# Performance work log

Measured on AMD Instinct MI355X. Metric: run time of the kernel, lower is better.

The kernel has to match this reference:

```python
import math
import jax, jax.numpy as jnp
import numpy as np

EPS = 1e-5

def lstm(x, Wih, Whh, b):
    # x: [N,T,D]; PyTorch gate order i,f,g,o; b = b_ih + b_hh combined
    N = x.shape[0]
    H = Whh.shape[1]
    gx = jnp.einsum('ntd,gd->ntg', x, Wih) + b  # [N,T,4H]
    def step(carry, g):
        h, c = carry
        z = g + h @ Whh.T
        i, f, gg, o = jnp.split(z, 4, axis=-1)
        c = jax.nn.sigmoid(f) * c + jax.nn.sigmoid(i) * jnp.tanh(gg)
        h = jax.nn.sigmoid(o) * jnp.tanh(c)
        return (h, c), h
    init = (jnp.zeros((N, H), x.dtype), jnp.zeros((N, H), x.dtype))
    (hN, _), ys = jax.lax.scan(step, init, jnp.swapaxes(gx, 0, 1))
    return jnp.swapaxes(ys, 0, 1), hN  # outputs [N,T,H], h_n [N,H]

def bilstm_layer(x, fW, fU, fb, bW, bU, bb):
    of, _ = lstm(x, fW, fU, fb)
    ob, _ = lstm(x[:, ::-1], bW, bU, bb)
    return jnp.concatenate([of, ob[:, ::-1]], axis=-1)

def layernorm(x, g, b):
    m = jnp.mean(x, -1, keepdims=True)
    v = jnp.mean((x - m) ** 2, -1, keepdims=True)
    return (x - m) * jax.lax.rsqrt(v + EPS) * g + b

def encoder_layer(src, Wq, bq, Wk, bk, Wv, bv, Wo, bo, W1, b1, W2, b2, lng, lnb):
    B, S, d = src.shape
    G, NH = 5, 5
    dk = d // NH
    # group channel shuffle (as in source)
    qs = src.reshape(B, S, G, d // G).swapaxes(-1, -2).reshape(B, S, d)
    q = qs @ Wq.T + bq
    k = q @ Wk.T + bk   # NOTE: source applies W_k/W_v to the projected query
    v = q @ Wv.T + bv
    def heads(t):
        return t.reshape(B, S, NH, dk).transpose(0, 2, 1, 3)
    qh, kh, vh = heads(q), heads(k), heads(v)
    attn = jax.nn.softmax(jnp.einsum('bhqd,bhkd->bhqk', qh, kh) / math.sqrt(dk), axis=-1)
    o = jnp.einsum('bhqk,bhkd->bhqd', attn, vh).transpose(0, 2, 1, 3).reshape(B, S, d)
    o = o @ Wo.T + bo
    src = layernorm(src + o, lng, lnb)          # dropout is identity in eval
    ff = jax.nn.relu(src @ W1.T + b1) @ W2.T + b2
    src = layernorm(src + ff, lng, lnb)         # same LayerNorm params reused
    return src, attn

def _forward(x, qWih, qWhh, qb, kWih, kWhh, kb, vWih, vWhh, vb,
             tWq, tbq, tWk, tbk, tWv, tbv, tWo, tbo, tW1, tb1, tW2, tb2, tlng, tlnb,
             l0fWih, l0fWhh, l0fb, l0bWih, l0bWhh, l0bb,
             l1fWih, l1fWhh, l1fb, l1bWih, l1bWhh, l1bb,
             fc1W, fc1b, fc2W, fc2b):
    B, T, F = x.shape
    H = qWhh.shape[1]
    # per-feature LSTMs: shared weights across features -> batch them
    xf = x.transpose(0, 2, 1).reshape(B * F, T, 1)
    _, hq = lstm(xf, qWih, qWhh, qb)   # [B*F,H]
    _, hk = lstm(xf, kWih, kWhh, kb)   # [B*F,H]
    _, hv = lstm(xf, vWih, vWhh, vb)   # [B*F,1]
    Q = hq.reshape(B, F, H)
    K = hk.reshape(B, F, H)
    V = hv.reshape(B, F)
    # b_ij = (q_i . k_j)/sqrt(H) * v_j, softmax over j
    scores = jnp.einsum('bih,bjh->bij', Q, K) / math.sqrt(H) * V[:, None, :]
    Wsm = jax.nn.softmax(scores, axis=-1)          # [B,F,F] rows indexed by i
    attn_output = jnp.einsum('btj,bij->bti', x, Wsm)  # bmm(x, softmax_b_i)
    b = Wsm.transpose(0, 2, 1)                     # stack(b_list, dim=-1)
    src = jnp.concatenate([x, attn_output], axis=-1)  # [B,T,2F]
    attns = []
    for l in range(2):
        src, a = encoder_layer(src, tWq[l], tbq[l], tWk[l], tbk[l], tWv[l], tbv[l],
                               tWo[l], tbo[l], tW1[l], tb1[l], tW2[l], tb2[l],
                               tlng[l], tlnb[l])
        attns.append(a)
    c = jnp.stack(attns)                           # [2,B,5,T,T]
    out = bilstm_layer(src, l0fWih, l0fWhh, l0fb, l0bWih, l0bWhh, l0bb)
    out = bilstm_layer(out, l1fWih, l1fWhh, l1fb, l1bWih, l1bWhh, l1bb)
    out = jax.nn.relu(out[:, -1, :])               # [B,2H]
    out = jax.nn.relu(out @ fc1W.T + fc1b)
    out = out @ fc2W.T + fc2b                      # [B,1]
    return out, b, c

def setup_inputs() -> dict:
    B, T, F, H = 16, 128, 40, 64
    d = 2 * F
    key = jax.random.key(0)
    ks = iter(jax.random.split(key, 64))
    def n(shape, fan):
        return (jax.random.normal(next(ks), shape) / math.sqrt(fan)).astype(jnp.float32)
    inp = {'x': jax.random.normal(next(ks), (B, T, F), dtype=jnp.float32)}
    # per-feature LSTMs
    inp.update(qWih=n((4 * H, 1), 1), qWhh=n((4 * H, H), H), qb=n((4 * H,), H))
    inp.update(kWih=n((4 * H, 1), 1), kWhh=n((4 * H, H), H), kb=n((4 * H,), H))
    inp.update(vWih=n((4, 1), 1), vWhh=n((4, 1), 1), vb=n((4,), 1))
    # transformer (2 layers stacked on leading axis)
    inp.update(tWq=n((2, d, d), d), tbq=n((2, d), d), tWk=n((2, d, d), d), tbk=n((2, d), d),
               tWv=n((2, d, d), d), tbv=n((2, d), d), tWo=n((2, d, d), d), tbo=n((2, d), d),
               tW1=n((2, 4 * d, d), d), tb1=n((2, 4 * d), d), tW2=n((2, d, 4 * d), 4 * d),
               tb2=n((2, d), 4 * d), tlng=jnp.ones((2, d), jnp.float32), tlnb=jnp.zeros((2, d), jnp.float32))
    # main bidirectional 2-layer LSTM
    inp.update(l0fWih=n((4 * H, d), d), l0fWhh=n((4 * H, H), H), l0fb=n((4 * H,), H),
               l0bWih=n((4 * H, d), d), l0bWhh=n((4 * H, H), H), l0bb=n((4 * H,), H),
               l1fWih=n((4 * H, 2 * H), 2 * H), l1fWhh=n((4 * H, H), H), l1fb=n((4 * H,), H),
               l1bWih=n((4 * H, 2 * H), 2 * H), l1bWhh=n((4 * H, H), H), l1bb=n((4 * H,), H))
    inp.update(fc1W=n((H, 2 * H), 2 * H), fc1b=n((H,), 2 * H), fc2W=n((1, H), H), fc2b=n((1,), H))
    return inp

def reference(x, qWih, qWhh, qb, kWih, kWhh, kb, vWih, vWhh, vb,
              tWq, tbq, tWk, tbk, tWv, tbv, tWo, tbo, tW1, tb1, tW2, tb2, tlng, tlnb,
              l0fWih, l0fWhh, l0fb, l0bWih, l0bWhh, l0bb,
              l1fWih, l1fWhh, l1fb, l1bWih, l1bWhh, l1bb,
              fc1W, fc1b, fc2W, fc2b):
    return _forward(x, qWih, qWhh, qb, kWih, kWhh, kb, vWih, vWhh, vb,
                    tWq, tbq, tWk, tbk, tWv, tbv, tWo, tbo, tW1, tb1, tW2, tb2, tlng, tlnb,
                    l0fWih, l0fWhh, l0fb, l0bWih, l0bWhh, l0bb,
                    l1fWih, l1fWhh, l1fb, l1bWih, l1bWhh, l1bb,
                    fc1W, fc1b, fc2W, fc2b)
```

## Files before the change

### kernel.cpp

```cpp
#include <hip/hip_runtime.h>

__device__ __forceinline__ float sigf(float x){ return 1.0f/(1.0f+__expf(-x)); }
__device__ __forceinline__ float tanhfast(float x){ return 1.0f - 2.0f/(__expf(2.0f*x)+1.0f); }

#define Bn 16
#define Tn 128
#define Fn 40
#define Hn 64
#define Dn 80
#define NHn 5
#define DKn 16
#define FFn 320

#define LOAD_PIN_ROW(dst, srcp)                                        \
  {                                                                    \
    _Pragma("unroll")                                                  \
    for (int jj=0; jj<16; ++jj){                                       \
      float4 tv = *(const float4*)((srcp) + 4*jj);                     \
      dst[4*jj]=tv.x; dst[4*jj+1]=tv.y; dst[4*jj+2]=tv.z; dst[4*jj+3]=tv.w; \
    }                                                                  \
    _Pragma("unroll")                                                  \
    for (int jj=0; jj<64; ++jj){ asm volatile("" : "+v"(dst[jj])); }   \
  }

#define LD4(p,i) (((const float4*)(p))[i])
#define DECL8(v, p) \
  float4 v##0=LD4(p,0), v##1=LD4(p,1), v##2=LD4(p,2), v##3=LD4(p,3), \
         v##4=LD4(p,4), v##5=LD4(p,5), v##6=LD4(p,6), v##7=LD4(p,7);
#define PIN4(P) asm volatile("" : "+v"(P.x), "+v"(P.y), "+v"(P.z), "+v"(P.w));
#define PIN8(v) PIN4(v##0) PIN4(v##1) PIN4(v##2) PIN4(v##3) PIN4(v##4) PIN4(v##5) \
  PIN4(v##6) PIN4(v##7)
#define ACC8(base) \
  { const float4 h0=hb4[(base)+0]; a += h0.x*w0.x + h0.y*w0.y + h0.z*w0.z + h0.w*w0.w; } \
  { const float4 h1=hb4[(base)+1]; a += h1.x*w1.x + h1.y*w1.y + h1.z*w1.z + h1.w*w1.w; } \
  { const float4 h2=hb4[(base)+2]; a += h2.x*w2.x + h2.y*w2.y + h2.z*w2.z + h2.w*w2.w; } \
  { const float4 h3=hb4[(base)+3]; a += h3.x*w3.x + h3.y*w3.y + h3.z*w3.z + h3.w*w3.w; } \
  { const float4 h4=hb4[(base)+4]; a += h4.x*w4.x + h4.y*w4.y + h4.z*w4.z + h4.w*w4.w; } \
  { const float4 h5=hb4[(base)+5]; a += h5.x*w5.x + h5.y*w5.y + h5.z*w5.z + h5.w*w5.w; } \
  { const float4 h6=hb4[(base)+6]; a += h6.x*w6.x + h6.y*w6.y + h6.z*w6.z + h6.w*w6.w; } \
  { const float4 h7=hb4[(base)+7]; a += h7.x*w7.x + h7.y*w7.y + h7.z*w7.z + h7.w*w7.w; }

__global__ __launch_bounds__(128,1) void k_feat_lstm2(
    const float* __restrict__ x,
    const float* __restrict__ qWih, const float* __restrict__ qWhh, const float* __restrict__ qb,
    const float* __restrict__ kWih, const float* __restrict__ kWhh, const float* __restrict__ kb,
    const float* __restrict__ vWih, const float* __restrict__ vWhh, const float* __restrict__ vb,
    float* __restrict__ hq, float* __restrict__ hk, float* __restrict__ hv)
{
  const int blk = blockIdx.x;
  const int l = threadIdx.x;
  if (blk >= 1280){
    const int inst = (blk - 1280)*128 + l;
    const int bi = inst/Fn, f = inst%Fn;
    const float* xp = x + bi*Tn*Fn + f;
    const float wih0=vWih[0], wih1=vWih[1], wih2=vWih[2], wih3=vWih[3];
    const float u0=vWhh[0], u1=vWhh[1], u2=vWhh[2], u3=vWhh[3];
    const float c0=vb[0], c1=vb[1], c2=vb[2], c3=vb[3];
    float h=0.f, c=0.f;
    #pragma unroll 1
    for (int t=0;t<Tn;++t){
      float xt = xp[t*Fn];
      float zi = xt*wih0 + h*u0 + c0;
      float zf = xt*wih1 + h*u1 + c1;
      float zg = xt*wih2 + h*u2 + c2;
      float zo = xt*wih3 + h*u3 + c3;
      c = sigf(zf)*c + sigf(zi)*tanhfast(zg);
      h = sigf(zo)*tanhfast(c);
    }
    hv[inst] = h;
    return;
  }
  const bool isk = blk >= 640;
  const int inst = isk ? blk-640 : blk;
  const int bi = inst/Fn, f = inst%Fn;
  const float* Whh = isk ? kWhh : qWhh;
  const float* Wih = isk ? kWih : qWih;
  const float* bia = isk ? kb  : qb;
  float* outp = isk ? hk : hq;

  const int r0 = l;
  const int r1 = l + 128;

  float w0[Hn], w1[Hn];
  LOAD_PIN_ROW(w0, Whh + r0*Hn);
  LOAD_PIN_ROW(w1, Whh + r1*Hn);
  const float wih0 = Wih[r0], wih1 = Wih[r1];
  const float bb0 = bia[r0], bb1 = bia[r1];

  __shared__ __align__(16) float hb[Hn];
  __shared__ float zb[4*Hn];
  __shared__ float xls[Tn];

  const float* xp = x + bi*Tn*Fn + f;
  xls[l] = xp[l*Fn];
  if (l < Hn) hb[l] = 0.f;
  float c = 0.f, h = 0.f;
  __syncthreads();

  const float4* hb4 = (const float4*)hb;
  #pragma unroll 1
  for (int t=0;t<Tn;++t){
    const float xt = xls[t];
    float a0 = bb0 + xt*wih0;
    float a1 = bb1 + xt*wih1;
    #pragma unroll
    for (int jj=0; jj<16; ++jj){
      const float4 hv4 = hb4[jj];
      a0 += hv4.x*w0[4*jj  ] + hv4.y*w0[4*jj+1] + hv4.z*w0[4*jj+2] + hv4.w*w0[4*jj+3];
      a1 += hv4.x*w1[4*jj  ] + hv4.y*w1[4*jj+1] + hv4.z*w1[4*jj+2] + hv4.w*w1[4*jj+3];
    }
    if (l >= Hn){ zb[l] = a0; zb[l+128] = a1; }
    __syncthreads();
    if (l < Hn){
      const float zi = a0, zg = a1;
      const float zf = zb[l+64], zo = zb[l+192];
      c = sigf(zf)*c + sigf(zi)*tanhfast(zg);
      h = sigf(zo)*tanhfast(c);
      hb[l] = h;
    }
    __syncthreads();
  }
  if (l < Hn) outp[inst*Hn + l] = h;
}

__global__ __launch_bounds__(64) void k_featattn(
    const float* __restrict__ hq, const float* __restrict__ hk, const float* __restrict__ hv,
    float* __restrict__ Wsm, float* __restrict__ out_b)
{
  const int blk = blockIdx.x;
  const int bi = blk / Fn, i = blk % Fn;
  const int j = threadIdx.x;
  __shared__ float qrow[Hn];
  qrow[j] = hq[blk*Hn + j];
  __syncthreads();
  float s = -1e30f;
  if (j < Fn){
    const float* krow = hk + (bi*Fn + j)*Hn;
    float a = 0.f;
    #pragma unroll
    for (int h2=0; h2<Hn; ++h2) a += qrow[h2]*krow[h2];
    s = a * 0.125f * hv[bi*Fn + j];
  }
  float m = s;
  #pragma unroll
  for (int off=32; off>0; off>>=1) m = fmaxf(m, __shfl_xor(m, off));
  float e = (j < Fn) ? __expf(s - m) : 0.f;
  float tot = e;
  #pragma unroll
  for (int off=32; off>0; off>>=1) tot += __shfl_xor(tot, off);
  float p = e / tot;
  if (j < Fn){
    Wsm[blk*Fn + j] = p;
    out_b[bi*(Fn*Fn) + j*Fn + i] = p;
  }
}

__global__ __launch_bounds__(128) void k_build_src(
    const float* __restrict__ x, const float* __restrict__ Wsm, float* __restrict__ src)
{
  const int blk = blockIdx.x;
  const int bi = blk / Tn;
  const int tid = threadIdx.x;
  __shared__ float xrow[Fn];
  if (tid < Fn) xrow[tid] = x[blk*Fn + tid];
  __syncthreads();
  if (tid < Fn){
    src[blk*Dn + tid] = xrow[tid];
  } else if (tid < Dn){
    const int i = tid - Fn;
    const float* wrow = Wsm + (bi*Fn + i)*Fn;
    float a = 0.f;
    #pragma unroll
    for (int j2=0;j2<Fn;++j2) a += xrow[j2]*wrow[j2];
    src[blk*Dn + tid] = a;
  }
}

__global__ __launch_bounds__(128) void k_qkv(
    const float* __restrict__ src,
    const float* __restrict__ Wq, const float* __restrict__ bq,
    const float* __restrict__ Wk, const float* __restrict__ bk,
    const float* __restrict__ Wv, const float* __restrict__ bv,
    float* __restrict__ q, float* __restrict__ k, float* __restrict__ v)
{
  const int row = blockIdx.x;
  const int t = threadIdx.x;
  __shared__ float qs[Dn];
  __shared__ float qrow[Dn];
  if (t < Dn) qs[t] = src[row*Dn + (t%5)*16 + t/5];
  __syncthreads();
  if (t < Dn){
    const float* wr = Wq + t*Dn;
    float a = bq[t];
    #pragma unroll 8
    for (int d2=0; d2<Dn; ++d2) a += qs[d2]*wr[d2];
    qrow[t] = a;
    q[row*Dn + t] = a;
  }
  __syncthreads();
  if (t < Dn){
    const float* wk = Wk + t*Dn;
    const float* wv = Wv + t*Dn;
    float ak = bk[t], av = bv[t];
    #pragma unroll 8
    for (int d2=0; d2<Dn; ++d2){ float qq = qrow[d2]; ak += qq*wk[d2]; av += qq*wv[d2]; }
    k[row*Dn + t] = ak;
    v[row*Dn + t] = av;
  }
}

__global__ __launch_bounds__(128) void k_attn(
    const float* __restrict__ q, const float* __restrict__ k, const float* __restrict__ v,
    float* __restrict__ o, float* __restrict__ c_out)
{
  const int s1 = blockIdx.x, h = blockIdx.y, bi = blockIdx.z;
  const int s2 = threadIdx.x;
  __shared__ float qf[DKn];
  __shared__ float p[Tn];
  __shared__ float pa[128];
  __shared__ float red_m[2];
  __shared__ float red_s[2];
  if (s2 < DKn) qf[s2] = q[(bi*Tn + s1)*Dn + h*DKn + s2];
  __syncthreads();
  const float* krow = k + (bi*Tn + s2)*Dn + h*DKn;
  float a = 0.f;
  #pragma unroll
  for (int d2=0; d2<DKn; ++d2) a += qf[d2]*krow[d2];
  a *= 0.25f;
  const int wv_id = s2 >> 6;
  float m = a;
  #pragma unroll
  for (int off=32; off>0; off>>=1) m = fmaxf(m, __shfl_xor(m, off));
  if ((s2 & 63) == 0) red_m[wv_id] = m;
  __syncthreads();
  m = fmaxf(red_m[0], red_m[1]);
  float e = __expf(a - m);
  float tot = e;
  #pragma unroll
  for (int off=32; off>0; off>>=1) tot += __shfl_xor(tot, off);
  if ((s2 & 63) == 0) red_s[wv_id] = tot;
  __syncthreads();
  tot = red_s[0] + red_s[1];
  float pv = e / tot;
  p[s2] = pv;
  c_out[((bi*NHn + h)*Tn + s1)*Tn + s2] = pv;
  __syncthreads();
  {
    const int d    = s2 & 15;
    const int part = s2 >> 4;
    const float* vcol = v + bi*Tn*Dn + h*DKn + d;
    float acc = 0.f;
    #pragma unroll
    for (int jj=0; jj<16; ++jj){
      const int j2 = part*16 + jj;
      acc += p[j2]*vcol[j2*Dn];
    }
    pa[s2] = acc;
  }
  __syncthreads();
  if (s2 < DKn){
    float acc = 0.f;
    #pragma unroll
    for (int k2=0; k2<8; ++k2) acc += pa[k2*16 + s2];
    o[(bi*Tn + s1)*Dn + h*DKn + s2] = acc;
  }
}

__global__ __launch_bounds__(320) void k_oln_ffln(
    const float* __restrict__ o, const float* __restrict__ Wo, const float* __restrict__ bo,
    const float* __restrict__ W1, const float* __restrict__ b1,
    const float* __restrict__ W2, const float* __restrict__ b2,
    const float* __restrict__ lng, const float* __restrict__ lnb, float* __restrict__ src)
{
  const int row = blockIdx.x;
  const int t = threadIdx.x;
  __shared__ float orow[Dn];
  __shared__ float s1row[Dn];
  __shared__ float h1[FFn];
  __shared__ float red[128];
  if (t < Dn) orow[t] = o[row*Dn + t];
  __syncthreads();
  float val = 0.f;
  if (t < Dn){
    const float* wr = Wo + t*Dn;
    float a = bo[t];
    #pragma unroll 8
    for (int d2=0; d2<Dn; ++d2) a += orow[d2]*wr[d2];
    val = a + src[row*Dn + t];
  }
  if (t < 128) red[t] = (t < Dn) ? val : 0.f;
  __syncthreads();
  for (int s=64; s>0; s>>=1){ if (t < s) red[t] += red[t+s]; __syncthreads(); }
  float mean = red[0] * (1.f/Dn);
  __syncthreads();
  if (t < 128){ float dv = (t < Dn) ? (val - mean) : 0.f; red[t] = dv*dv; }
  __syncthreads();
  for (int s=64; s>0; s>>=1){ if (t < s) red[t] += red[t+s]; __syncthreads(); }
  float rstd = rsqrtf(red[0]*(1.f/Dn) + 1e-5f);
  if (t < Dn) s1row[t] = (val - mean)*rstd*lng[t] + lnb[t];
  __syncthreads();
  {
    const float* wr = W1 + t*Dn;
    float a = b1[t];
    #pragma unroll 8
    for (int d2=0; d2<Dn; ++d2) a += s1row[d2]*wr[d2];
    h1[t] = fmaxf(a, 0.f);
  }
  __syncthreads();
  float val2 = 0.f;
  if (t < Dn){
    const float* wr = W2 + t*FFn;
    float a = b2[t];
    #pragma unroll 8
    for (int d2=0; d2<FFn; ++d2) a += h1[d2]*wr[d2];
    val2 = a + s1row[t];
  }
  if (t < 128) red[t] = (t < Dn) ? val2 : 0.f;
  __syncthreads();
  for (int s=64; s>0; s>>=1){ if (t < s) red[t] += red[t+s]; __syncthreads(); }
  mean = red[0] * (1.f/Dn);
  __syncthreads();
  if (t < 128){ float dv = (t < Dn) ? (val2 - mean) : 0.f; red[t] = dv*dv; }
  __syncthreads();
  for (int s=64; s>0; s>>=1){ if (t < s) red[t] += red[t+s]; __syncthreads(); }
  rstd = rsqrtf(red[0]*(1.f/Dn) + 1e-5f);
  if (t < Dn) src[row*Dn + t] = (val2 - mean)*rstd*lng[t] + lnb[t];
}

template<int IND>
__global__ __launch_bounds__(256) void k_gx8(
    const float* __restrict__ X,
    const float* __restrict__ WihF, const float* __restrict__ bF,
    const float* __restrict__ WihB, const float* __restrict__ bB,
    float* __restrict__ gx)
{
  const int row0 = blockIdx.x * 8;
  const int dir = blockIdx.y;
  const int g = threadIdx.x;
  __shared__ float xs[8][IND];
  #pragma unroll
  for (int rr=0; rr<8; ++rr)
    for (int d2=g; d2<IND; d2+=256) xs[rr][d2] = X[(row0+rr)*IND + d2];
  __syncthreads();
  const float* W  = dir ? WihB : WihF;
  const float* bb = dir ? bB  : bF;
  const float* wr = W + g*IND;
  float acc[8];
  const float b0 = bb[g];
  #pragma unroll
  for (int rr=0; rr<8; ++rr) acc[rr] = b0;
  #pragma unroll 4
  for (int d2=0; d2<IND; d2+=4){
    const float4 wv = *(const float4*)(wr + d2);
    #pragma unroll
    for (int rr=0; rr<8; ++rr){
      acc[rr] += xs[rr][d2]*wv.x + xs[rr][d2+1]*wv.y + xs[rr][d2+2]*wv.z + xs[rr][d2+3]*wv.w;
    }
  }
  float* gxd = gx + dir*(Bn*Tn*256);
  #pragma unroll
  for (int rr=0; rr<8; ++rr) gxd[(row0+rr)*256 + g] = acc[rr];
}

__global__ __launch_bounds__(512)
void k_bilstm_rec5(
    const float* __restrict__ gx,
    const float* __restrict__ WhhF, const float* __restrict__ WhhB,
    float* __restrict__ outp)
{
  const int n = blockIdx.x;
  const int dir = blockIdx.y;
  const int t = threadIdx.x;
  const int half = t >> 8;
  const int r    = t & 255;
  const float* Whh = dir ? WhhB : WhhF;
  DECL8(w, Whh + r*Hn + half*32);
  PIN8(w);

  __shared__ __align__(16) float hb[Hn];
  __shared__ float pa[512];
  if (t < Hn) hb[t] = 0.f;
  float c = 0.f, h = 0.f;
  __syncthreads();

  const float* gxd = gx + dir*(Bn*Tn*256) + n*Tn*256;
  const float4* hb4 = (const float4*)hb;
  const int jbase = half*8;
  const int t0 = dir ? Tn-1 : 0;
  float g0 = half ? 0.f : gxd[t0*256 + r];
  #pragma unroll 1
  for (int step=0; step<Tn; ++step){
    const int tt = dir ? (Tn-1-step) : step;
    int tn = dir ? (Tn-2-step) : (step+1);
    tn = max(0, min(Tn-1, tn));
    const float p0 = half ? 0.f : gxd[tn*256 + r];
    float a = g0;
    ACC8(jbase)
    pa[t] = a;
    __syncthreads();
    if (t < Hn){
      const float zi = pa[t    ] + pa[t+256];
      const float zf = pa[t+ 64] + pa[t+320];
      const float zg = pa[t+128] + pa[t+384];
      const float zo = pa[t+192] + pa[t+448];
      c = sigf(zf)*c + sigf(zi)*tanhfast(zg);
      h = sigf(zo)*tanhfast(c);
      hb[t] = h;
      outp[(n*Tn + tt)*128 + dir*Hn + t] = h;
    }
    __syncthreads();
    g0 = p0;
  }
}

__global__ __launch_bounds__(128) void k_final(
    const float* __restrict__ out1,
    const float* __restrict__ fc1W, const float* __restrict__ fc1b,
    const float* __restrict__ fc2W, const float* __restrict__ fc2b,
    float* __restrict__ outp)
{
  const int n = blockIdx.x;
  const int t = threadIdx.x;
  __shared__ float r[128];
  __shared__ float a1[64];
  r[t] = fmaxf(out1[(n*Tn + (Tn-1))*128 + t], 0.f);
  __syncthreads();
  if (t < 64){
    const float* wr = fc1W + t*128;
    float a = fc1b[t];
    #pragma unroll 8
    for (int d2=0; d2<128; ++d2) a += r[d2]*wr[d2];
    a1[t] = fmaxf(a, 0.f);
  }
  __syncthreads();
  if (t == 0){
    float a = fc2b[0];
    #pragma unroll 8
    for (int d2=0; d2<64; ++d2) a += a1[d2]*fc2W[d2];
    outp[n] = a;
  }
}

extern "C" void kernel_launch(void* const* d_in, const int* in_sizes, int n_in,
                              void* d_out, int out_size, void* d_ws, size_t ws_size,
                              hipStream_t stream)
{
  const float* x     = (const float*)d_in[0];
  const float* qWih  = (const float*)d_in[1];
  const float* qWhh  = (const float*)d_in[2];
  const float* qb    = (const float*)d_in[3];
  const float* kWih  = (const float*)d_in[4];
  const float* kWhh  = (const float*)d_in[5];
  const float* kb    = (const float*)d_in[6];
  const float* vWih  = (const float*)d_in[7];
  const float* vWhh  = (const float*)d_in[8];
  const float* vb    = (const float*)d_in[9];
  const float* tWq   = (const float*)d_in[10];
  const float* tbq   = (const float*)d_in[11];
  const float* tWk   = (const float*)d_in[12];
  const float* tbk   = (const float*)d_in[13];
  const float* tWv   = (const float*)d_in[14];
  const float* tbv   = (const float*)d_in[15];
  const float* tWo   = (const float*)d_in[16];
  const float* tbo   = (const float*)d_in[17];
  const float* tW1   = (const float*)d_in[18];
  const float* tb1   = (const float*)d_in[19];
  const float* tW2   = (const float*)d_in[20];
  const float* tb2   = (const float*)d_in[21];
  const float* tlng  = (const float*)d_in[22];
  const float* tlnb  = (const float*)d_in[23];
  const float* l0fWih= (const float*)d_in[24];
  const float* l0fWhh= (const float*)d_in[25];
  const float* l0fb  = (const float*)d_in[26];
  const float* l0bWih= (const float*)d_in[27];
  const float* l0bWhh= (const float*)d_in[28];
  const float* l0bb  = (const float*)d_in[29];
  const float* l1fWih= (const float*)d_in[30];
  const float* l1fWhh= (const float*)d_in[31];
  const float* l1fb  = (const float*)d_in[32];
  const float* l1bWih= (const float*)d_in[33];
  const float* l1bWhh= (const float*)d_in[34];
  const float* l1bb  = (const float*)d_in[35];
  const float* fc1W  = (const float*)d_in[36];
  const float* fc1b  = (const float*)d_in[37];
  const float* fc2W  = (const float*)d_in[38];
  const float* fc2b  = (const float*)d_in[39];

  float* ws  = (float*)d_ws;
  float* hq  = ws;
  float* hk  = hq  + 640*64;
  float* hv  = hk  + 640*64;
  float* Wsm = hv  + 640;
  float* src = Wsm + 16*40*40;
  float* q   = src + 16*128*80;
  float* k   = q   + 16*128*80;
  float* v   = k   + 16*128*80;
  float* o   = v   + 16*128*80;
  float* gx  = o   + 16*128*80;
  float* lout0 = gx + 2*16*128*256;
  float* lout1 = lout0 + 16*128*128;

  float* outp  = (float*)d_out;
  float* out_b = outp + 16;
  float* out_c = out_b + 16*40*40;

  k_feat_lstm2<<<1285, 128, 0, stream>>>(x, qWih,qWhh,qb, kWih,kWhh,kb, vWih,vWhh,vb, hq,hk,hv);
  k_featattn<<<640, 64, 0, stream>>>(hq, hk, hv, Wsm, out_b);
  k_build_src<<<2048, 128, 0, stream>>>(x, Wsm, src);
  for (int l=0; l<2; ++l){
    k_qkv<<<2048, 128, 0, stream>>>(src, tWq + l*Dn*Dn, tbq + l*Dn,
                                    tWk + l*Dn*Dn, tbk + l*Dn,
                                    tWv + l*Dn*Dn, tbv + l*Dn, q, k, v);
    k_attn<<<dim3(128,5,16), 128, 0, stream>>>(q, k, v, o, out_c + (size_t)l*16*5*128*128);
    k_oln_ffln<<<2048, 320, 0, stream>>>(o, tWo + l*Dn*Dn, tbo + l*Dn,
                                         tW1 + l*FFn*Dn, tb1 + l*FFn,
                                         tW2 + l*Dn*FFn, tb2 + l*Dn,
                                         tlng + l*Dn, tlnb + l*Dn, src);
  }
  k_gx8<80><<<dim3(256,2), 256, 0, stream>>>(src, l0fWih, l0fb, l0bWih, l0bb, gx);
  k_bilstm_rec5<<<dim3(16,2), 512, 0, stream>>>(gx, l0fWhh, l0bWhh, lout0);
  k_gx8<128><<<dim3(256,2), 256, 0, stream>>>(lout0, l1fWih, l1fb, l1bWih, l1bb, gx);
  k_bilstm_rec5<<<dim3(16,2), 512, 0, stream>>>(gx, l1fWhh, l1bWhh, lout1);
  k_final<<<16, 128, 0, stream>>>(lout1, fc1W, fc1b, fc2W, fc2b, outp);
}
```

Before: 663.1 us.

## Batch multiple sequences per block in feature and bidirectional LSTM recurrences

The per-feature LSTM kernel now processes 8 (batch, feature) instances per 256-thread block, with one gate row per thread, instead of one instance per 128-thread block. The main BiLSTM recurrence kernel now handles 2 sequences per 256-thread block instead of 1 sequence per 512-thread block with a split dot product. The aim is to reuse each weight row across several sequences and cut the number of blocks. In exchange, weights that were pinned in registers are now reloaded from memory every timestep. Each thread also does more serial work per step, which lengthens the latency-bound critical path.

```diff
diff --git a/kernel.cpp b/kernel.cpp
--- a/kernel.cpp
+++ b/kernel.cpp
@@ -12,35 +12,7 @@
 #define DKn 16
 #define FFn 320
 
-#define LOAD_PIN_ROW(dst, srcp)                                        \
-  {                                                                    \
-    _Pragma("unroll")                                                  \
-    for (int jj=0; jj<16; ++jj){                                       \
-      float4 tv = *(const float4*)((srcp) + 4*jj);                     \
-      dst[4*jj]=tv.x; dst[4*jj+1]=tv.y; dst[4*jj+2]=tv.z; dst[4*jj+3]=tv.w; \
-    }                                                                  \
-    _Pragma("unroll")                                                  \
-    for (int jj=0; jj<64; ++jj){ asm volatile("" : "+v"(dst[jj])); }   \
-  }
-
-#define LD4(p,i) (((const float4*)(p))[i])
-#define DECL8(v, p) \
-  float4 v##0=LD4(p,0), v##1=LD4(p,1), v##2=LD4(p,2), v##3=LD4(p,3), \
-         v##4=LD4(p,4), v##5=LD4(p,5), v##6=LD4(p,6), v##7=LD4(p,7);
-#define PIN4(P) asm volatile("" : "+v"(P.x), "+v"(P.y), "+v"(P.z), "+v"(P.w));
-#define PIN8(v) PIN4(v##0) PIN4(v##1) PIN4(v##2) PIN4(v##3) PIN4(v##4) PIN4(v##5) \
-  PIN4(v##6) PIN4(v##7)
-#define ACC8(base) \
-  { const float4 h0=hb4[(base)+0]; a += h0.x*w0.x + h0.y*w0.y + h0.z*w0.z + h0.w*w0.w; } \
-  { const float4 h1=hb4[(base)+1]; a += h1.x*w1.x + h1.y*w1.y + h1.z*w1.z + h1.w*w1.w; } \
-  { const float4 h2=hb4[(base)+2]; a += h2.x*w2.x + h2.y*w2.y + h2.z*w2.z + h2.w*w2.w; } \
-  { const float4 h3=hb4[(base)+3]; a += h3.x*w3.x + h3.y*w3.y + h3.z*w3.z + h3.w*w3.w; } \
-  { const float4 h4=hb4[(base)+4]; a += h4.x*w4.x + h4.y*w4.y + h4.z*w4.z + h4.w*w4.w; } \
-  { const float4 h5=hb4[(base)+5]; a += h5.x*w5.x + h5.y*w5.y + h5.z*w5.z + h5.w*w5.w; } \
-  { const float4 h6=hb4[(base)+6]; a += h6.x*w6.x + h6.y*w6.y + h6.z*w6.z + h6.w*w6.w; } \
-  { const float4 h7=hb4[(base)+7]; a += h7.x*w7.x + h7.y*w7.y + h7.z*w7.z + h7.w*w7.w; }
-
-__global__ __launch_bounds__(128,1) void k_feat_lstm2(
+__global__ __launch_bounds__(256) void k_feat_b8(
     const float* __restrict__ x,
     const float* __restrict__ qWih, const float* __restrict__ qWhh, const float* __restrict__ qb,
     const float* __restrict__ kWih, const float* __restrict__ kWhh, const float* __restrict__ kb,
@@ -48,79 +20,91 @@
     float* __restrict__ hq, float* __restrict__ hk, float* __restrict__ hv)
 {
   const int blk = blockIdx.x;
-  const int l = threadIdx.x;
-  if (blk >= 1280){
-    const int inst = (blk - 1280)*128 + l;
-    const int bi = inst/Fn, f = inst%Fn;
-    const float* xp = x + bi*Tn*Fn + f;
-    const float wih0=vWih[0], wih1=vWih[1], wih2=vWih[2], wih3=vWih[3];
-    const float u0=vWhh[0], u1=vWhh[1], u2=vWhh[2], u3=vWhh[3];
-    const float c0=vb[0], c1=vb[1], c2=vb[2], c3=vb[3];
-    float h=0.f, c=0.f;
-    #pragma unroll 1
-    for (int t=0;t<Tn;++t){
-      float xt = xp[t*Fn];
-      float zi = xt*wih0 + h*u0 + c0;
-      float zf = xt*wih1 + h*u1 + c1;
-      float zg = xt*wih2 + h*u2 + c2;
-      float zo = xt*wih3 + h*u3 + c3;
-      c = sigf(zf)*c + sigf(zi)*tanhfast(zg);
-      h = sigf(zo)*tanhfast(c);
-    }
-    hv[inst] = h;
+  const int t = threadIdx.x;
+  if (blk >= 160){
+    const int inst = (blk - 160)*256 + t;
+    if (inst < 640){
+      const int bi = inst/Fn, f = inst%Fn;
+      const float* xp = x + bi*Tn*Fn + f;
+      const float wih0=vWih[0], wih1=vWih[1], wih2=vWih[2], wih3=vWih[3];
+      const float u0v=vWhh[0], u1v=vWhh[1], u2v=vWhh[2], u3v=vWhh[3];
+      const float c0=vb[0], c1=vb[1], c2=vb[2], c3=vb[3];
+      float h=0.f, c=0.f;
+      #pragma unroll 1
+      for (int tt=0;tt<Tn;++tt){
+        float xt = xp[tt*Fn];
+        float zi = xt*wih0 + h*u0v + c0;
+        float zf = xt*wih1 + h*u1v + c1;
+        float zg = xt*wih2 + h*u2v + c2;
+        float zo = xt*wih3 + h*u3v + c3;
+        c = sigf(zf)*c + sigf(zi)*tanhfast(zg);
+        h = sigf(zo)*tanhfast(c);
+      }
+      hv[inst] = h;
+    }
     return;
   }
-  const bool isk = blk >= 640;
-  const int inst = isk ? blk-640 : blk;
-  const int bi = inst/Fn, f = inst%Fn;
+  const bool isk = blk >= 80;
+  const int grp = isk ? blk-80 : blk;
+  const int inst0 = grp*8;
   const float* Whh = isk ? kWhh : qWhh;
   const float* Wih = isk ? kWih : qWih;
   const float* bia = isk ? kb  : qb;
   float* outp = isk ? hk : hq;
 
-  const int r0 = l;
-  const int r1 = l + 128;
-
-  float w0[Hn], w1[Hn];
-  LOAD_PIN_ROW(w0, Whh + r0*Hn);
-  LOAD_PIN_ROW(w1, Whh + r1*Hn);
-  const float wih0 = Wih[r0], wih1 = Wih[r1];
-  const float bb0 = bia[r0], bb1 = bia[r1];
-
-  __shared__ __align__(16) float hb[Hn];
-  __shared__ float zb[4*Hn];
-  __shared__ float xls[Tn];
-
-  const float* xp = x + bi*Tn*Fn + f;
-  xls[l] = xp[l*Fn];
-  if (l < Hn) hb[l] = 0.f;
-  float c = 0.f, h = 0.f;
-  __syncthreads();
-
-  const float4* hb4 = (const float4*)hb;
+  const float4* wr4 = (const float4*)(Whh + t*Hn);
+  const float wih = Wih[t];
+  const float bb  = bia[t];
+
+  __shared__ __align__(16) float hls[8*Hn];
+  __shared__ float zls[8*256];
+  __shared__ float xls[8*Tn];
+
+  for (int idx=t; idx<8*Tn; idx+=256){
+    const int g = idx >> 7, tt = idx & 127;
+    const int inst = inst0 + g;
+    const int bi = inst/Fn, f = inst%Fn;
+    xls[idx] = x[(bi*Tn+tt)*Fn + f];
+  }
+  for (int idx=t; idx<8*Hn; idx+=256) hls[idx] = 0.f;
+  float c0 = 0.f, c1 = 0.f;
+  __syncthreads();
+
+  const float4* hls4 = (const float4*)hls;
+  const int gA = t >> 6, hiA = t & 63;
+  const int gB = 4 + (t >> 6), hiB = t & 63;
+
   #pragma unroll 1
-  for (int t=0;t<Tn;++t){
-    const float xt = xls[t];
-    float a0 = bb0 + xt*wih0;
-    float a1 = bb1 + xt*wih1;
+  for (int tt=0; tt<Tn; ++tt){
+    float a[8];
+    #pragma unroll
+    for (int g=0; g<8; ++g) a[g] = bb + xls[g*Tn + tt]*wih;
     #pragma unroll
     for (int jj=0; jj<16; ++jj){
-      const float4 hv4 = hb4[jj];
-      a0 += hv4.x*w0[4*jj  ] + hv4.y*w0[4*jj+1] + hv4.z*w0[4*jj+2] + hv4.w*w0[4*jj+3];
-      a1 += hv4.x*w1[4*jj  ] + hv4.y*w1[4*jj+1] + hv4.z*w1[4*jj+2] + hv4.w*w1[4*jj+3];
-    }
-    if (l >= Hn){ zb[l] = a0; zb[l+128] = a1; }
+      const float4 wv = wr4[jj];
+      #pragma unroll
+      for (int g=0; g<8; ++g){
+        const float4 hv = hls4[g*16 + jj];
+        a[g] += hv.x*wv.x + hv.y*wv.y + hv.z*wv.z + hv.w*wv.w;
+      }
+    }
+    #pragma unroll
+    for (int g=0; g<8; ++g) zls[g*256 + t] = a[g];
     __syncthreads();
-    if (l < Hn){
-      const float zi = a0, zg = a1;
-      const float zf = zb[l+64], zo = zb[l+192];
-      c = sigf(zf)*c + sigf(zi)*tanhfast(zg);
-      h = sigf(zo)*tanhfast(c);
-      hb[l] = h;
+    {
+      float zi=zls[gA*256+hiA], zf=zls[gA*256+64+hiA], zg=zls[gA*256+128+hiA], zo=zls[gA*256+192+hiA];
+      c0 = sigf(zf)*c0 + sigf(zi)*tanhfast(zg);
+      hls[gA*Hn + hiA] = sigf(zo)*tanhfast(c0);
+      zi=zls[gB*256+hiB]; zf=zls[gB*256+64+hiB]; zg=zls[gB*256+128+hiB]; zo=zls[gB*256+192+hiB];
+      c1 = sigf(zf)*c1 + sigf(zi)*tanhfast(zg);
+      hls[gB*Hn + hiB] = sigf(zo)*tanhfast(c1);
     }
     __syncthreads();
   }
-  if (l < Hn) outp[inst*Hn + l] = h;
+  for (int idx=t; idx<8*Hn; idx+=256){
+    const int g = idx >> 6, hi = idx & 63;
+    outp[(inst0+g)*Hn + hi] = hls[g*Hn + hi];
+  }
 }
 
 __global__ __launch_bounds__(64) void k_featattn(
@@ -362,54 +346,61 @@
   for (int rr=0; rr<8; ++rr) gxd[(row0+rr)*256 + g] = acc[rr];
 }
 
-__global__ __launch_bounds__(512)
-void k_bilstm_rec5(
+__global__ __launch_bounds__(256) void k_rec_b2(
     const float* __restrict__ gx,
     const float* __restrict__ WhhF, const float* __restrict__ WhhB,
     float* __restrict__ outp)
 {
-  const int n = blockIdx.x;
+  const int nb = blockIdx.x;
   const int dir = blockIdx.y;
   const int t = threadIdx.x;
-  const int half = t >> 8;
-  const int r    = t & 255;
   const float* Whh = dir ? WhhB : WhhF;
-  DECL8(w, Whh + r*Hn + half*32);
-  PIN8(w);
-
-  __shared__ __align__(16) float hb[Hn];
-  __shared__ float pa[512];
-  if (t < Hn) hb[t] = 0.f;
-  float c = 0.f, h = 0.f;
-  __syncthreads();
-
-  const float* gxd = gx + dir*(Bn*Tn*256) + n*Tn*256;
-  const float4* hb4 = (const float4*)hb;
-  const int jbase = half*8;
+  const float4* wr4 = (const float4*)(Whh + t*Hn);
+
+  __shared__ __align__(16) float hls[2*Hn];
+  __shared__ float zls[2*256];
+  for (int idx=t; idx<2*Hn; idx+=256) hls[idx] = 0.f;
+  float cst = 0.f;
+  __syncthreads();
+
+  const float4* hls4 = (const float4*)hls;
+  const float* gxd = gx + dir*(Bn*Tn*256);
   const int t0 = dir ? Tn-1 : 0;
-  float g0 = half ? 0.f : gxd[t0*256 + r];
+  float g0 = gxd[((nb*2+0)*Tn + t0)*256 + t];
+  float g1 = gxd[((nb*2+1)*Tn + t0)*256 + t];
+  const int gact = t >> 6, hiact = t & 63;
+
   #pragma unroll 1
   for (int step=0; step<Tn; ++step){
     const int tt = dir ? (Tn-1-step) : step;
     int tn = dir ? (Tn-2-step) : (step+1);
     tn = max(0, min(Tn-1, tn));
-    const float p0 = half ? 0.f : gxd[tn*256 + r];
-    float a = g0;
-    ACC8(jbase)
-    pa[t] = a;
+    const float p0 = gxd[((nb*2+0)*Tn + tn)*256 + t];
+    const float p1 = gxd[((nb*2+1)*Tn + tn)*256 + t];
+    float a0 = g0, a1 = g1;
+    #pragma unroll
+    for (int jj=0; jj<16; ++jj){
+      const float4 wv = wr4[jj];
+      const float4 h0 = hls4[jj];
+      const float4 h1 = hls4[16 + jj];
+      a0 += h0.x*wv.x + h0.y*wv.y + h0.z*wv.z + h0.w*wv.w;
+      a1 += h1.x*wv.x + h1.y*wv.y + h1.z*wv.z + h1.w*wv.w;
+    }
+    zls[t] = a0;
+    zls[256 + t] = a1;
     __syncthreads();
-    if (t < Hn){
-      const float zi = pa[t    ] + pa[t+256];
-      const float zf = pa[t+ 64] + pa[t+320];
-      const float zg = pa[t+128] + pa[t+384];
-      const float zo = pa[t+192] + pa[t+448];
-      c = sigf(zf)*c + sigf(zi)*tanhfast(zg);
-      h = sigf(zo)*tanhfast(c);
-      hb[t] = h;
-      outp[(n*Tn + tt)*128 + dir*Hn + t] = h;
+    if (t < 128){
+      const float zi = zls[gact*256 + hiact];
+      const float zf = zls[gact*256 + 64 + hiact];
+      const float zg = zls[gact*256 + 128 + hiact];
+      const float zo = zls[gact*256 + 192 + hiact];
+      cst = sigf(zf)*cst + sigf(zi)*tanhfast(zg);
+      const float hnew = sigf(zo)*tanhfast(cst);
+      hls[gact*Hn + hiact] = hnew;
+      outp[((nb*2+gact)*Tn + tt)*128 + dir*Hn + hiact] = hnew;
     }
     __syncthreads();
-    g0 = p0;
+    g0 = p0; g1 = p1;
   }
 }
 
@@ -504,7 +495,7 @@
   float* out_b = outp + 16;
   float* out_c = out_b + 16*40*40;
 
-  k_feat_lstm2<<<1285, 128, 0, stream>>>(x, qWih,qWhh,qb, kWih,kWhh,kb, vWih,vWhh,vb, hq,hk,hv);
+  k_feat_b8<<<163, 256, 0, stream>>>(x, qWih,qWhh,qb, kWih,kWhh,kb, vWih,vWhh,vb, hq,hk,hv);
   k_featattn<<<640, 64, 0, stream>>>(hq, hk, hv, Wsm, out_b);
   k_build_src<<<2048, 128, 0, stream>>>(x, Wsm, src);
   for (int l=0; l<2; ++l){
@@ -518,8 +509,8 @@
                                          tlng + l*Dn, tlnb + l*Dn, src);
   }
   k_gx8<80><<<dim3(256,2), 256, 0, stream>>>(src, l0fWih, l0fb, l0bWih, l0bb, gx);
-  k_bilstm_rec5<<<dim3(16,2), 512, 0, stream>>>(gx, l0fWhh, l0bWhh, lout0);
+  k_rec_b2<<<dim3(8,2), 256, 0, stream>>>(gx, l0fWhh, l0bWhh, lout0);
   k_gx8<128><<<dim3(256,2), 256, 0, stream>>>(lout0, l1fWih, l1fb, l1bWih, l1bb, gx);
-  k_bilstm_rec5<<<dim3(16,2), 512, 0, stream>>>(gx, l1fWhh, l1bWhh, lout1);
+  k_rec_b2<<<dim3(8,2), 256, 0, stream>>>(gx, l1fWhh, l1bWhh, lout1);
   k_final<<<16, 128, 0, stream>>>(lout1, fc1W, fc1b, fc2W, fc2b, outp);
 }
```

Measured after the change: 1.297 ms. 95.6% more time.

## Batch two feature-LSTM instances per block to reuse register-resident weights

Applied to the files above, without the earlier changes.

Each block of the per-feature q/k LSTM kernel now handles two (batch,feature) instances instead of one, reusing the same register-pinned Whh rows for both hidden-state vectors. The grid is roughly halved and all 128 threads now do the gate nonlinearities, instead of only 64. This amortises weight loading and per-step barrier overhead across two sequences, at the cost of more shared memory, more live registers, and fewer blocks in flight.

```diff
diff --git a/kernel.cpp b/kernel.cpp
--- a/kernel.cpp
+++ b/kernel.cpp
@@ -40,7 +40,7 @@
   { const float4 h6=hb4[(base)+6]; a += h6.x*w6.x + h6.y*w6.y + h6.z*w6.z + h6.w*w6.w; } \
   { const float4 h7=hb4[(base)+7]; a += h7.x*w7.x + h7.y*w7.y + h7.z*w7.z + h7.w*w7.w; }
 
-__global__ __launch_bounds__(128,1) void k_feat_lstm2(
+__global__ __launch_bounds__(128,1) void k_feat_g2(
     const float* __restrict__ x,
     const float* __restrict__ qWih, const float* __restrict__ qWhh, const float* __restrict__ qb,
     const float* __restrict__ kWih, const float* __restrict__ kWhh, const float* __restrict__ kb,
@@ -49,8 +49,8 @@
 {
   const int blk = blockIdx.x;
   const int l = threadIdx.x;
-  if (blk >= 1280){
-    const int inst = (blk - 1280)*128 + l;
+  if (blk >= 640){
+    const int inst = (blk - 640)*128 + l;
     const int bi = inst/Fn, f = inst%Fn;
     const float* xp = x + bi*Tn*Fn + f;
     const float wih0=vWih[0], wih1=vWih[1], wih2=vWih[2], wih3=vWih[3];
@@ -70,9 +70,9 @@
     hv[inst] = h;
     return;
   }
-  const bool isk = blk >= 640;
-  const int inst = isk ? blk-640 : blk;
-  const int bi = inst/Fn, f = inst%Fn;
+  const bool isk = blk >= 320;
+  const int grp = isk ? blk-320 : blk;
+  const int inst0 = grp*2;
   const float* Whh = isk ? kWhh : qWhh;
   const float* Wih = isk ? kWih : qWih;
   const float* bia = isk ? kb  : qb;
@@ -87,40 +87,56 @@
   const float wih0 = Wih[r0], wih1 = Wih[r1];
   const float bb0 = bia[r0], bb1 = bia[r1];
 
-  __shared__ __align__(16) float hb[Hn];
-  __shared__ float zb[4*Hn];
-  __shared__ float xls[Tn];
-
-  const float* xp = x + bi*Tn*Fn + f;
-  xls[l] = xp[l*Fn];
-  if (l < Hn) hb[l] = 0.f;
+  __shared__ __align__(16) float hb[2*Hn];
+  __shared__ float zb[2][4*Hn];
+  __shared__ float xls[2*Tn];
+
+  {
+    const int bi0 = inst0/Fn, f0 = inst0%Fn;
+    const int bi1 = (inst0+1)/Fn, f1 = (inst0+1)%Fn;
+    xls[l]      = x[(bi0*Tn+l)*Fn + f0];
+    xls[Tn + l] = x[(bi1*Tn+l)*Fn + f1];
+  }
+  if (l < 2*Hn) hb[l] = 0.f;
   float c = 0.f, h = 0.f;
   __syncthreads();
 
   const float4* hb4 = (const float4*)hb;
+  const int gact = l >> 6;
+  const int hact = l & 63;
+
   #pragma unroll 1
   for (int t=0;t<Tn;++t){
-    const float xt = xls[t];
-    float a0 = bb0 + xt*wih0;
-    float a1 = bb1 + xt*wih1;
+    float a00 = bb0 + xls[t]*wih0;
+    float a01 = bb1 + xls[t]*wih1;
+    float a10 = bb0 + xls[Tn+t]*wih0;
+    float a11 = bb1 + xls[Tn+t]*wih1;
     #pragma unroll
     for (int jj=0; jj<16; ++jj){
-      const float4 hv4 = hb4[jj];
-      a0 += hv4.x*w0[4*jj  ] + hv4.y*w0[4*jj+1] + hv4.z*w0[4*jj+2] + hv4.w*w0[4*jj+3];
-      a1 += hv4.x*w1[4*jj  ] + hv4.y*w1[4*jj+1] + hv4.z*w1[4*jj+2] + hv4.w*w1[4*jj+3];
+      const float4 h0 = hb4[jj];
+      const float4 h1 = hb4[16 + jj];
+      const float wa = w0[4*jj], wb = w0[4*jj+1], wc = w0[4*jj+2], wd = w0[4*jj+3];
+      a00 += h0.x*wa + h0.y*wb + h0.z*wc + h0.w*wd;
+      a10 += h1.x*wa + h1.y*wb + h1.z*wc + h1.w*wd;
+      const float ua = w1[4*jj], ub = w1[4*jj+1], uc = w1[4*jj+2], ud = w1[4*jj+3];
+      a01 += h0.x*ua + h0.y*ub + h0.z*uc + h0.w*ud;
+      a11 += h1.x*ua + h1.y*ub + h1.z*uc + h1.w*ud;
     }
-    if (l >= Hn){ zb[l] = a0; zb[l+128] = a1; }
+    zb[0][r0] = a00; zb[0][r1] = a01;
+    zb[1][r0] = a10; zb[1][r1] = a11;
     __syncthreads();
-    if (l < Hn){
-      const float zi = a0, zg = a1;
-      const float zf = zb[l+64], zo = zb[l+192];
+    {
+      const float zi = zb[gact][hact];
+      const float zf = zb[gact][hact+64];
+      const float zg = zb[gact][hact+128];
+      const float zo = zb[gact][hact+192];
       c = sigf(zf)*c + sigf(zi)*tanhfast(zg);
       h = sigf(zo)*tanhfast(c);
-      hb[l] = h;
+      hb[gact*Hn + hact] = h;
     }
     __syncthreads();
   }
-  if (l < Hn) outp[inst*Hn + l] = h;
+  outp[(inst0+gact)*Hn + hact] = h;
 }
 
 __global__ __launch_bounds__(64) void k_featattn(
@@ -504,7 +520,7 @@
   float* out_b = outp + 16;
   float* out_c = out_b + 16*40*40;
 
-  k_feat_lstm2<<<1285, 128, 0, stream>>>(x, qWih,qWhh,qb, kWih,kWhh,kb, vWih,vWhh,vb, hq,hk,hv);
+  k_feat_g2<<<645, 128, 0, stream>>>(x, qWih,qWhh,qb, kWih,kWhh,kb, vWih,vWhh,vb, hq,hk,hv);
   k_featattn<<<640, 64, 0, stream>>>(hq, hk, hv, Wsm, out_b);
   k_build_src<<<2048, 128, 0, stream>>>(x, Wsm, src);
   for (int l=0; l<2; ++l){
```

Result: slower. 752.7 us (+13.5%).
